# Kernel tuning notes

Hardware: AMD Instinct MI355X
Metric: run time of the kernel (lower is better)

Reference implementation:

```python
import jax, jax.numpy as jnp
import numpy as np

B, S, H = 2, 2048, 2048
NH = 16
Q_LORA, KV_LORA = 1536, 512
D_NOPE, D_ROPE, D_V = 128, 64, 128
D_QK = D_NOPE + D_ROPE
SCALE = 1.0 / np.sqrt(D_QK)
EPS = 1e-6


def _freqs(seq_len):
    # precompute_freqs_cis with scaling_factor=1.0 -> plain RoPE
    inv = 1.0 / (10000.0 ** (np.arange(0, D_ROPE, 2, dtype=np.float32) / D_ROPE))
    t = np.arange(seq_len, dtype=np.float32)
    f = np.outer(t, inv)  # (S, D_ROPE//2)
    return jnp.asarray(np.cos(f)), jnp.asarray(np.sin(f))


def _rope_interleaved(x, cos, sin):
    # x: (B, S, heads, D_ROPE); cos/sin: (S, D_ROPE//2)
    b, s, h, d = x.shape
    xr = x.reshape(b, s, h, d // 2, 2)
    e, o = xr[..., 0], xr[..., 1]
    c = cos[None, :, None, :]
    sn = sin[None, :, None, :]
    re = e * c - o * sn
    im = e * sn + o * c
    return jnp.stack([re, im], axis=-1).reshape(b, s, h, d)


def _rmsnorm(x, w):
    xf = x.astype(jnp.float32)
    rms = jnp.sqrt(jnp.mean(xf * xf, axis=-1, keepdims=True) + EPS)
    return (w * (xf / rms)).astype(x.dtype)


def setup_inputs() -> dict:
    key = jax.random.key(0)
    ks = jax.random.split(key, 6)
    def w(k, shape, fan_in):
        return jax.random.normal(k, shape, dtype=jnp.float32) * (1.0 / np.sqrt(fan_in))
    return {
        "hidden_states": jax.random.normal(ks[0], (B, S, H), dtype=jnp.float32),
        "wq_a": w(ks[1], (Q_LORA, H), H),
        "q_norm_w": jnp.ones((Q_LORA,), dtype=jnp.float32),
        "wq_b": w(ks[2], (NH * D_QK, Q_LORA), Q_LORA),
        "wkv_a": w(ks[3], (KV_LORA + D_ROPE, H), H),
        "kv_norm_w": jnp.ones((KV_LORA,), dtype=jnp.float32),
        "wkv_b": w(ks[4], (NH * (D_NOPE + D_V), KV_LORA), KV_LORA),
        "wo": w(ks[5], (H, NH * D_V), NH * D_V),
    }


def reference(hidden_states, wq_a, q_norm_w, wq_b, wkv_a, kv_norm_w, wkv_b, wo):
    b, s, _ = hidden_states.shape
    cos, sin = _freqs(s)

    # low-rank Q path
    q = hidden_states @ wq_a.T                      # (B,S,Q_LORA)
    q = _rmsnorm(q, q_norm_w)
    q = (q @ wq_b.T).reshape(b, s, NH, D_QK)        # (B,S,NH,192)
    q_nope, q_pe = q[..., :D_NOPE], q[..., D_NOPE:]

    # joint KV compression
    kv = hidden_states @ wkv_a.T                    # (B,S,KV_LORA+D_ROPE)
    kv_c, k_pe = kv[..., :KV_LORA], kv[..., KV_LORA:]
    kv_c = _rmsnorm(kv_c, kv_norm_w)
    k_pe = _rope_interleaved(k_pe[:, :, None, :], cos, sin)  # (B,S,1,64)

    kv_x = (kv_c @ wkv_b.T).reshape(b, s, NH, D_NOPE + D_V)
    k_nope, v = kv_x[..., :D_NOPE], kv_x[..., D_NOPE:]

    q_pe = _rope_interleaved(q_pe, cos, sin)
    qf = jnp.concatenate([q_nope, q_pe], axis=-1)   # (B,S,NH,192)
    kf = jnp.concatenate([k_nope, jnp.broadcast_to(k_pe, (b, s, NH, D_ROPE))], axis=-1)

    scores = jnp.einsum("bqhd,bkhd->bhqk", qf, kf) * SCALE
    attn = jax.nn.softmax(scores.astype(jnp.float32), axis=-1).astype(qf.dtype)
    out = jnp.einsum("bhqk,bkhd->bqhd", attn, v).reshape(b, s, NH * D_V)
    return out @ wo.T
```

## Files before the change

### kernel.cpp

```cpp
#include <hip/hip_runtime.h>
#include <math.h>

#define B_   2
#define S_   2048
#define H_   2048
#define NH_  16
#define T_   (B_*S_)
#define QL   1536
#define KVL  512
#define DN   128
#define DR   64
#define DQK  192
#define DV   128
#define SCALE_ 0.07216878364870323f
#define EPS_ 1e-6f
#define NQKV 2176

typedef unsigned short u16;
typedef __attribute__((ext_vector_type(8))) short bf16x8;
typedef __attribute__((ext_vector_type(4))) float f32x4;

__device__ __forceinline__ u16 f2b(float x) {
  union { float f; unsigned u; } v; v.f = x;
  unsigned r = v.u + 0x7FFFu + ((v.u >> 16) & 1u);
  return (u16)(r >> 16);
}
__device__ __forceinline__ float b2f(u16 u) {
  union { unsigned u; float f; } v; v.u = ((unsigned)u) << 16; return v.f;
}

#define GLD16(src, dst) __builtin_amdgcn_global_load_lds(                       \
    (const __attribute__((address_space(1))) unsigned int*)(src),               \
    (__attribute__((address_space(3))) unsigned int*)(dst), 16, 0, 0)

__device__ __forceinline__ void cvt4(const float* in, u16* out, int i) {
  float4 v = ((const float4*)in)[i];
  u16 r[4] = {f2b(v.x), f2b(v.y), f2b(v.z), f2b(v.w)};
  ((uint2*)out)[i] = *(uint2*)r;
}

__global__ __launch_bounds__(256) void cvt_all(
    const float* __restrict__ hid, const float* __restrict__ wqa,
    const float* __restrict__ wqb, const float* __restrict__ wkva,
    const float* __restrict__ wkvb, const float* __restrict__ wo,
    u16* __restrict__ o_hid, u16* __restrict__ o_wqa, u16* __restrict__ o_wqb,
    u16* __restrict__ o_wkva, u16* __restrict__ o_wkvb, u16* __restrict__ o_wo) {
  int i = blockIdx.x * 256 + threadIdx.x;
  if (i < 2097152) { cvt4(hid, o_hid, i); return; }
  i -= 2097152;
  if (i < 786432) { cvt4(wqa, o_wqa, i); return; }
  i -= 786432;
  if (i < 1179648) { cvt4(wqb, o_wqb, i); return; }
  i -= 1179648;
  if (i < 327680) {
    int row = i >> 9;
    u16 r[4] = {0, 0, 0, 0};
    if (row < 576) {
      float4 v = ((const float4*)wkva)[i];
      r[0] = f2b(v.x); r[1] = f2b(v.y); r[2] = f2b(v.z); r[3] = f2b(v.w);
    }
    ((uint2*)o_wkva)[i] = *(uint2*)r;
    return;
  }
  i -= 327680;
  if (i < 524288) { cvt4(wkvb, o_wkvb, i); return; }
  i -= 524288;
  if (i < 1048576) cvt4(wo, o_wo, i);
}

template <int OUTMODE>
__global__ __launch_bounds__(256) void gemm_mfma(
    const u16* __restrict__ A, int lda,
    const u16* __restrict__ W, int ldw,
    float* __restrict__ Cf, u16* __restrict__ Cb, int ldc,
    int K, float outscale) {
  __shared__ u16 As[4096];
  __shared__ u16 Bs[4096];
  const int tid = threadIdx.x;
  const int wave = tid >> 6, lane = tid & 63, quad = lane >> 4, l16 = lane & 15;
  const int wm = (wave >> 1) * 64, wn = (wave & 1) * 64;
  const size_t m0 = (size_t)blockIdx.y * 128, n0 = (size_t)blockIdx.x * 128;

  f32x4 acc[4][4];
#pragma unroll
  for (int i = 0; i < 4; ++i)
#pragma unroll
    for (int j = 0; j < 4; ++j) acc[i][j] = (f32x4){0.f, 0.f, 0.f, 0.f};

  const int g0 = tid, g1 = tid + 256;
  const u16* a0 = A + (m0 + (g0 >> 6) * 16 + (g0 & 15)) * (size_t)lda + ((g0 >> 4) & 3) * 8;
  const u16* a1 = A + (m0 + (g1 >> 6) * 16 + (g1 & 15)) * (size_t)lda + ((g1 >> 4) & 3) * 8;
  const u16* b0 = W + (n0 + (g0 >> 6) * 16 + (g0 & 15)) * (size_t)ldw + ((g0 >> 4) & 3) * 8;
  const u16* b1 = W + (n0 + (g1 >> 6) * 16 + (g1 & 15)) * (size_t)ldw + ((g1 >> 4) & 3) * 8;

  for (int k0 = 0; k0 < K; k0 += 32) {
    __syncthreads();
    GLD16(a0 + k0, &As[g0 * 8]);
    GLD16(a1 + k0, &As[g1 * 8]);
    GLD16(b0 + k0, &Bs[g0 * 8]);
    GLD16(b1 + k0, &Bs[g1 * 8]);
    __syncthreads();

    bf16x8 af[4], bfr[4];
#pragma unroll
    for (int i = 0; i < 4; ++i)
      af[i] = *(const bf16x8*)&As[((wm >> 4) + i) * 512 + quad * 128 + l16 * 8];
#pragma unroll
    for (int j = 0; j < 4; ++j)
      bfr[j] = *(const bf16x8*)&Bs[((wn >> 4) + j) * 512 + quad * 128 + l16 * 8];
#pragma unroll
    for (int i = 0; i < 4; ++i)
#pragma unroll
      for (int j = 0; j < 4; ++j)
        acc[i][j] = __builtin_amdgcn_mfma_f32_16x16x32_bf16(af[i], bfr[j], acc[i][j], 0, 0, 0);
  }

#pragma unroll
  for (int i = 0; i < 4; ++i)
#pragma unroll
    for (int j = 0; j < 4; ++j)
#pragma unroll
      for (int r = 0; r < 4; ++r) {
        size_t m = m0 + wm + i * 16 + quad * 4 + r;
        size_t n = n0 + wn + j * 16 + l16;
        if (OUTMODE == 0) Cf[m * ldc + n] = acc[i][j][r];
        else              Cb[m * ldc + n] = f2b(acc[i][j][r] * outscale);
      }
}

__global__ __launch_bounds__(256) void rmsnorm_bf(
    const float* __restrict__ x, const float* __restrict__ w,
    u16* __restrict__ o, int D, int sx, int so) {
  const float* p = x + (size_t)blockIdx.x * sx;
  u16* q = o + (size_t)blockIdx.x * so;
  float ss = 0.f;
  for (int i = threadIdx.x; i < D; i += 256) { float v = p[i]; ss += v * v; }
#pragma unroll
  for (int off = 32; off; off >>= 1) ss += __shfl_down(ss, off);
  __shared__ float red[4];
  __shared__ float s_inv;
  if ((threadIdx.x & 63) == 0) red[threadIdx.x >> 6] = ss;
  __syncthreads();
  if (threadIdx.x == 0) {
    float t = red[0] + red[1] + red[2] + red[3];
    s_inv = 1.0f / sqrtf(t / (float)D + EPS_);
  }
  __syncthreads();
  float inv = s_inv;
  for (int i = threadIdx.x; i < D; i += 256) q[i] = f2b(w[i] * p[i] * inv);
}

__global__ void rope_q_bf(u16* __restrict__ Q) {
  int idx = blockIdx.x * blockDim.x + threadIdx.x;
  int pair = idx & 31;
  int head = (idx >> 5) & (NH_ - 1);
  int row = idx >> 9;
  if (row >= T_) return;
  int s = row & (S_ - 1);
  float inv = powf(10000.0f, -(float)(2 * pair) * (1.0f / 64.0f));
  float ang = (float)s * inv;
  float c = cosf(ang), sn = sinf(ang);
  u16* p = Q + (size_t)row * (NH_ * DQK) + head * DQK + DN + 2 * pair;
  unsigned u = *(unsigned*)p;
  float e = b2f((u16)(u & 0xffff)), o = b2f((u16)(u >> 16));
  float re = e * c - o * sn;
  float im = e * sn + o * c;
  *(unsigned*)p = (unsigned)f2b(re) | ((unsigned)f2b(im) << 16);
}

__global__ void kpe_bf_kernel(const float* __restrict__ KVa, u16* __restrict__ KPE) {
  int idx = blockIdx.x * blockDim.x + threadIdx.x;
  int pair = idx & 31;
  int row = idx >> 5;
  if (row >= T_) return;
  int s = row & (S_ - 1);
  float inv = powf(10000.0f, -(float)(2 * pair) * (1.0f / 64.0f));
  float ang = (float)s * inv;
  float c = cosf(ang), sn = sinf(ang);
  const float* p = KVa + (size_t)row * NQKV + 2048 + 2 * pair;
  float e = p[0], o = p[1];
  float re = e * c - o * sn;
  float im = e * sn + o * c;
  *(unsigned*)(KPE + (size_t)row * 64 + 2 * pair) =
      (unsigned)f2b(re) | ((unsigned)f2b(im) << 16);
}

__global__ __launch_bounds__(256) void conv_vt(const u16* __restrict__ KVbf,
                                               u16* __restrict__ Vt) {
  const int h = blockIdx.y, b = blockIdx.z;
  const int s0 = (blockIdx.x >> 1) * 64, d0 = (blockIdx.x & 1) * 64;
  const int t0 = b * S_;
  __shared__ u16 tile[64][72];
  const int tid = threadIdx.x;
#pragma unroll
  for (int i = 0; i < 2; ++i) {
    int c = tid + i * 256;
    int row = c >> 3, off = (c & 7) * 8;
    *(uint4*)&tile[row][off] =
        *(const uint4*)(KVbf + (size_t)(t0 + s0 + row) * 4096 + h * 256 + 128 + d0 + off);
  }
  __syncthreads();
#pragma unroll
  for (int i = 0; i < 2; ++i) {
    int c = tid + i * 256;
    int drow = c >> 3, soff = (c & 7) * 8;
    u16 vals[8];
#pragma unroll
    for (int j = 0; j < 8; ++j) vals[j] = tile[soff + j][drow];
    *(uint4*)(Vt + ((size_t)(b * NH_ + h) * 128 + d0 + drow) * 2048 + s0 + soff) =
        *(uint4*)vals;
  }
}

__global__ __launch_bounds__(512, 4) void flash_mfma(
    const u16* __restrict__ Qbf,
    const u16* __restrict__ KVbf,
    const u16* __restrict__ KPE,
    const u16* __restrict__ Vt,
    u16* __restrict__ Out) {
  const int h = blockIdx.y, b = blockIdx.z;
  const int q0 = blockIdx.x * 128;
  const int t0 = b * S_;
  const int tid = threadIdx.x;
  const int wave = tid >> 6, lane = tid & 63, quad = lane >> 4, l16 = lane & 15;

  __shared__ u16 Ks[2][64 * 192];
  __shared__ u16 Vs[2][128 * 64];

  bf16x8 qf[6];
  {
    const u16* qp = Qbf + (size_t)(t0 + q0 + wave * 16 + l16) * (NH_ * DQK) + h * DQK + quad * 8;
#pragma unroll
    for (int c = 0; c < 6; ++c) qf[c] = *(const bf16x8*)(qp + c * 32);
  }

  const u16* kbase[3]; int kstep[3];
#pragma unroll
  for (int i = 0; i < 3; ++i) {
    int g = i * 512 + tid;
    int r = g & 15, cc = (g >> 4) % 24, kk = (g >> 4) / 24;
    int tok = kk * 16 + r;
    if (cc < 16) { kbase[i] = KVbf + (size_t)(t0 + tok) * 4096 + h * 256 + cc * 8; kstep[i] = 64 * 4096; }
    else         { kbase[i] = KPE + (size_t)(t0 + tok) * 64 + (cc - 16) * 8;       kstep[i] = 64 * 64; }
  }
  const u16* vbase[2];
#pragma unroll
  for (int i = 0; i < 2; ++i) {
    int g = i * 512 + tid;
    int r = g & 15, kc = (g >> 4) & 7, dt = g >> 7;
    vbase[i] = Vt + ((size_t)((b * NH_ + h) * 128) + dt * 16 + r) * 2048 + kc * 8;
  }

  f32x4 of[8];
#pragma unroll
  for (int i = 0; i < 8; ++i) of[i] = (f32x4){0.f, 0.f, 0.f, 0.f};
  float mrun = -3e38f, lrun = 0.f;

#pragma unroll
  for (int i = 0; i < 3; ++i) { GLD16(kbase[i], &Ks[0][(i * 512 + tid) * 8]); kbase[i] += kstep[i]; }
#pragma unroll
  for (int i = 0; i < 2; ++i) GLD16(vbase[i], &Vs[0][(i * 512 + tid) * 8]);

  const int src_lo = (quad & 1) * 32 + l16;
  const int src_hi = src_lo + 16;
  const bool hi_kk = (quad >> 1) != 0;

  for (int it = 0; it < S_ / 64; ++it) {
    const int cur = it & 1;
    __syncthreads();

    if (it + 1 < S_ / 64) {
#pragma unroll
      for (int i = 0; i < 3; ++i) { GLD16(kbase[i], &Ks[cur ^ 1][(i * 512 + tid) * 8]); kbase[i] += kstep[i]; }
#pragma unroll
      for (int i = 0; i < 2; ++i) GLD16(vbase[i] + (it + 1) * 64, &Vs[cur ^ 1][(i * 512 + tid) * 8]);
    }

    f32x4 sc[4];
#pragma unroll
    for (int kk = 0; kk < 4; ++kk) {
      f32x4 s = (f32x4){0.f, 0.f, 0.f, 0.f};
#pragma unroll
      for (int c = 0; c < 6; ++c) {
        bf16x8 kf = *(const bf16x8*)&Ks[cur][((kk * 24 + c * 4 + quad) * 16 + l16) * 8];
        s = __builtin_amdgcn_mfma_f32_16x16x32_bf16(kf, qf[c], s, 0, 0, 0);
      }
      sc[kk] = s;
    }

    float tm = sc[0][0];
#pragma unroll
    for (int kk = 0; kk < 4; ++kk)
#pragma unroll
      for (int r = 0; r < 4; ++r) tm = fmaxf(tm, sc[kk][r]);
    tm = fmaxf(tm, __shfl_xor(tm, 16, 64));
    tm = fmaxf(tm, __shfl_xor(tm, 32, 64));
    float mnew = fmaxf(mrun, tm);
    float alpha = __expf(mrun - mnew);
    mrun = mnew;
    float lsum = 0.f;
#pragma unroll
    for (int kk = 0; kk < 4; ++kk)
#pragma unroll
      for (int r = 0; r < 4; ++r) {
        float p = __expf(sc[kk][r] - mnew);
        sc[kk][r] = p;
        lsum += p;
      }
    lsum += __shfl_xor(lsum, 16, 64);
    lsum += __shfl_xor(lsum, 32, 64);
    lrun = lrun * alpha + lsum;

    unsigned pb[4][2];
#pragma unroll
    for (int kk = 0; kk < 4; ++kk) {
      pb[kk][0] = (unsigned)f2b(sc[kk][0]) | ((unsigned)f2b(sc[kk][1]) << 16);
      pb[kk][1] = (unsigned)f2b(sc[kk][2]) | ((unsigned)f2b(sc[kk][3]) << 16);
    }

    bf16x8 pa[2];
#pragma unroll
    for (int c2 = 0; c2 < 2; ++c2) {
      unsigned a0 = __shfl(pb[c2 * 2][0], src_lo, 64);
      unsigned b0 = __shfl(pb[c2 * 2 + 1][0], src_lo, 64);
      unsigned a1 = __shfl(pb[c2 * 2][1], src_lo, 64);
      unsigned b1 = __shfl(pb[c2 * 2 + 1][1], src_lo, 64);
      unsigned a2 = __shfl(pb[c2 * 2][0], src_hi, 64);
      unsigned b2 = __shfl(pb[c2 * 2 + 1][0], src_hi, 64);
      unsigned a3 = __shfl(pb[c2 * 2][1], src_hi, 64);
      unsigned b3 = __shfl(pb[c2 * 2 + 1][1], src_hi, 64);
      union { unsigned w[4]; bf16x8 v; } u;
      u.w[0] = hi_kk ? b0 : a0;
      u.w[1] = hi_kk ? b1 : a1;
      u.w[2] = hi_kk ? b2 : a2;
      u.w[3] = hi_kk ? b3 : a3;
      pa[c2] = u.v;
    }

#pragma unroll
    for (int dt = 0; dt < 8; ++dt) {
#pragma unroll
      for (int r = 0; r < 4; ++r) of[dt][r] *= alpha;
#pragma unroll
      for (int c2 = 0; c2 < 2; ++c2) {
        bf16x8 vf = *(const bf16x8*)&Vs[cur][((dt * 8 + c2 * 4 + quad) * 16 + l16) * 8];
        of[dt] = __builtin_amdgcn_mfma_f32_16x16x32_bf16(vf, pa[c2], of[dt], 0, 0, 0);
      }
    }
  }

  float inv = 1.0f / lrun;
  u16* op = Out + (size_t)(t0 + q0 + wave * 16 + l16) * (NH_ * DV) + h * DV + quad * 4;
#pragma unroll
  for (int dt = 0; dt < 8; ++dt) {
    u16 r4[4] = {f2b(of[dt][0] * inv), f2b(of[dt][1] * inv),
                 f2b(of[dt][2] * inv), f2b(of[dt][3] * inv)};
    *(uint2*)(op + dt * 16) = *(uint2*)r4;
  }
}

extern "C" void kernel_launch(void* const* d_in, const int* in_sizes, int n_in,
                              void* d_out, int out_size, void* d_ws, size_t ws_size,
                              hipStream_t stream) {
  const float* hidden  = (const float*)d_in[0];
  const float* wq_a    = (const float*)d_in[1];
  const float* q_norm  = (const float*)d_in[2];
  const float* wq_b    = (const float*)d_in[3];
  const float* wkv_a   = (const float*)d_in[4];
  const float* kv_norm = (const float*)d_in[5];
  const float* wkv_b   = (const float*)d_in[6];
  const float* wo      = (const float*)d_in[7];
  float* out = (float*)d_out;

  float* ws = (float*)d_ws;
  u16*   hid_bf  = (u16*)(ws);
  u16*   wqa_bf  = (u16*)(ws + 4194304);
  u16*   wkva_bf = (u16*)(ws + 5767168);
  u16*   wqb_bf  = (u16*)(ws + 6422528);
  u16*   wkvb_bf = (u16*)(ws + 8781824);
  u16*   wo_bf   = (u16*)(ws + 9830400);
  float* qkv_a   = ws + 11927552;
  u16*   attn_bf = (u16*)(ws + 11927552);
  u16*   vt      = (u16*)(ws + 16121856);
  u16*   q_bf    = (u16*)(ws + 22413312);
  u16*   kvn_bf  = (u16*)(ws + 28704768);
  u16*   kpe     = (u16*)(ws + 29753344);
  u16*   kv_bf   = (u16*)(ws + 29884416);
  u16*   qn_bf   = (u16*)(ws + 29884416);
  const size_t need = (size_t)38273024 * sizeof(float);
  if (ws_size < need) return;

  cvt_all<<<23296, 256, 0, stream>>>(hidden, wq_a, wq_b, wkv_a, wkv_b, wo,
                                     hid_bf, wqa_bf, wqb_bf, wkva_bf, wkvb_bf, wo_bf);

  gemm_mfma<0><<<dim3(NQKV / 128, T_ / 128), 256, 0, stream>>>(
      hid_bf, H_, wqa_bf, H_, qkv_a, nullptr, NQKV, H_, 1.0f);

  rmsnorm_bf<<<T_, 256, 0, stream>>>(qkv_a, q_norm, qn_bf, QL, NQKV, QL);
  gemm_mfma<1><<<dim3(NH_ * DQK / 128, T_ / 128), 256, 0, stream>>>(
      qn_bf, QL, wqb_bf, QL, nullptr, q_bf, NH_ * DQK, QL, SCALE_);
  rope_q_bf<<<T_ * NH_ * 32 / 256, 256, 0, stream>>>(q_bf);

  rmsnorm_bf<<<T_, 256, 0, stream>>>(qkv_a + QL, kv_norm, kvn_bf, KVL, NQKV, KVL);
  kpe_bf_kernel<<<T_ * 32 / 256, 256, 0, stream>>>(qkv_a, kpe);
  gemm_mfma<1><<<dim3(NH_ * (DN + DV) / 128, T_ / 128), 256, 0, stream>>>(
      kvn_bf, KVL, wkvb_bf, KVL, nullptr, kv_bf, NH_ * (DN + DV), KVL, 1.0f);
  conv_vt<<<dim3(64, NH_, B_), 256, 0, stream>>>(kv_bf, vt);

  flash_mfma<<<dim3(S_ / 128, NH_, B_), 512, 0, stream>>>(q_bf, kv_bf, kpe, vt, attn_bf);

  gemm_mfma<0><<<dim3(H_ / 128, T_ / 128), 256, 0, stream>>>(
      attn_bf, NH_ * DV, wo_bf, NH_ * DV, out, nullptr, H_, NH_ * DV, 1.0f);
}
```

Measured before the change: 573.1 us.

## Process two query sub-tiles per wave in flash attention with 256-thread blocks

The flash attention kernel now uses 4 waves per block instead of 8, and each wave handles two 16-row query sub-tiles (A and B). Every K and V fragment read from LDS feeds two MFMAs, which halves LDS read traffic per unit of compute. It also adds s_setprio around the MFMA sections and skips the output rescale when no lane's running max changed. The cost is more registers per wave, fewer waves to hide latency, and more global-to-LDS copies per thread.

```diff
diff --git a/kernel.cpp b/kernel.cpp
--- a/kernel.cpp
+++ b/kernel.cpp
@@ -212,7 +212,7 @@
   }
 }
 
-__global__ __launch_bounds__(512, 4) void flash_mfma(
+__global__ __launch_bounds__(256, 2) void flash_mfma(
     const u16* __restrict__ Qbf,
     const u16* __restrict__ KVbf,
     const u16* __restrict__ KPE,
@@ -227,39 +227,47 @@
   __shared__ u16 Ks[2][64 * 192];
   __shared__ u16 Vs[2][128 * 64];
 
-  bf16x8 qf[6];
+  bf16x8 qfA[6], qfB[6];
   {
-    const u16* qp = Qbf + (size_t)(t0 + q0 + wave * 16 + l16) * (NH_ * DQK) + h * DQK + quad * 8;
-#pragma unroll
-    for (int c = 0; c < 6; ++c) qf[c] = *(const bf16x8*)(qp + c * 32);
-  }
-
-  const u16* kbase[3]; int kstep[3];
-#pragma unroll
-  for (int i = 0; i < 3; ++i) {
-    int g = i * 512 + tid;
+    const u16* qpA = Qbf + (size_t)(t0 + q0 + wave * 32 + l16) * (NH_ * DQK) + h * DQK + quad * 8;
+    const u16* qpB = qpA + 16 * (NH_ * DQK);
+#pragma unroll
+    for (int c = 0; c < 6; ++c) {
+      qfA[c] = *(const bf16x8*)(qpA + c * 32);
+      qfB[c] = *(const bf16x8*)(qpB + c * 32);
+    }
+  }
+
+  const u16* kbase[6]; int kstep[6];
+#pragma unroll
+  for (int i = 0; i < 6; ++i) {
+    int g = i * 256 + tid;
     int r = g & 15, cc = (g >> 4) % 24, kk = (g >> 4) / 24;
     int tok = kk * 16 + r;
     if (cc < 16) { kbase[i] = KVbf + (size_t)(t0 + tok) * 4096 + h * 256 + cc * 8; kstep[i] = 64 * 4096; }
     else         { kbase[i] = KPE + (size_t)(t0 + tok) * 64 + (cc - 16) * 8;       kstep[i] = 64 * 64; }
   }
-  const u16* vbase[2];
-#pragma unroll
-  for (int i = 0; i < 2; ++i) {
-    int g = i * 512 + tid;
+  const u16* vbase[4];
+#pragma unroll
+  for (int i = 0; i < 4; ++i) {
+    int g = i * 256 + tid;
     int r = g & 15, kc = (g >> 4) & 7, dt = g >> 7;
     vbase[i] = Vt + ((size_t)((b * NH_ + h) * 128) + dt * 16 + r) * 2048 + kc * 8;
   }
 
-  f32x4 of[8];
-#pragma unroll
-  for (int i = 0; i < 8; ++i) of[i] = (f32x4){0.f, 0.f, 0.f, 0.f};
-  float mrun = -3e38f, lrun = 0.f;
-
-#pragma unroll
-  for (int i = 0; i < 3; ++i) { GLD16(kbase[i], &Ks[0][(i * 512 + tid) * 8]); kbase[i] += kstep[i]; }
-#pragma unroll
-  for (int i = 0; i < 2; ++i) GLD16(vbase[i], &Vs[0][(i * 512 + tid) * 8]);
+  f32x4 ofA[8], ofB[8];
+#pragma unroll
+  for (int i = 0; i < 8; ++i) {
+    ofA[i] = (f32x4){0.f, 0.f, 0.f, 0.f};
+    ofB[i] = (f32x4){0.f, 0.f, 0.f, 0.f};
+  }
+  float mrunA = -3e38f, lrunA = 0.f;
+  float mrunB = -3e38f, lrunB = 0.f;
+
+#pragma unroll
+  for (int i = 0; i < 6; ++i) { GLD16(kbase[i], &Ks[0][(i * 256 + tid) * 8]); kbase[i] += kstep[i]; }
+#pragma unroll
+  for (int i = 0; i < 4; ++i) GLD16(vbase[i], &Vs[0][(i * 256 + tid) * 8]);
 
   const int src_lo = (quad & 1) * 32 + l16;
   const int src_hi = src_lo + 16;
@@ -271,91 +279,170 @@
 
     if (it + 1 < S_ / 64) {
 #pragma unroll
-      for (int i = 0; i < 3; ++i) { GLD16(kbase[i], &Ks[cur ^ 1][(i * 512 + tid) * 8]); kbase[i] += kstep[i]; }
-#pragma unroll
-      for (int i = 0; i < 2; ++i) GLD16(vbase[i] + (it + 1) * 64, &Vs[cur ^ 1][(i * 512 + tid) * 8]);
-    }
-
-    f32x4 sc[4];
+      for (int i = 0; i < 6; ++i) { GLD16(kbase[i], &Ks[cur ^ 1][(i * 256 + tid) * 8]); kbase[i] += kstep[i]; }
+#pragma unroll
+      for (int i = 0; i < 4; ++i) GLD16(vbase[i] + (it + 1) * 64, &Vs[cur ^ 1][(i * 256 + tid) * 8]);
+    }
+
+    __builtin_amdgcn_s_setprio(1);
+    f32x4 scA[4], scB[4];
 #pragma unroll
     for (int kk = 0; kk < 4; ++kk) {
-      f32x4 s = (f32x4){0.f, 0.f, 0.f, 0.f};
+      f32x4 sA = (f32x4){0.f, 0.f, 0.f, 0.f};
+      f32x4 sB = (f32x4){0.f, 0.f, 0.f, 0.f};
 #pragma unroll
       for (int c = 0; c < 6; ++c) {
         bf16x8 kf = *(const bf16x8*)&Ks[cur][((kk * 24 + c * 4 + quad) * 16 + l16) * 8];
-        s = __builtin_amdgcn_mfma_f32_16x16x32_bf16(kf, qf[c], s, 0, 0, 0);
+        sA = __builtin_amdgcn_mfma_f32_16x16x32_bf16(kf, qfA[c], sA, 0, 0, 0);
+        sB = __builtin_amdgcn_mfma_f32_16x16x32_bf16(kf, qfB[c], sB, 0, 0, 0);
       }
-      sc[kk] = s;
-    }
-
-    float tm = sc[0][0];
+      scA[kk] = sA;
+      scB[kk] = sB;
+    }
+    __builtin_amdgcn_s_setprio(0);
+
+    float tmA = scA[0][0];
 #pragma unroll
     for (int kk = 0; kk < 4; ++kk)
 #pragma unroll
-      for (int r = 0; r < 4; ++r) tm = fmaxf(tm, sc[kk][r]);
-    tm = fmaxf(tm, __shfl_xor(tm, 16, 64));
-    tm = fmaxf(tm, __shfl_xor(tm, 32, 64));
-    float mnew = fmaxf(mrun, tm);
-    float alpha = __expf(mrun - mnew);
-    mrun = mnew;
-    float lsum = 0.f;
+      for (int r = 0; r < 4; ++r) tmA = fmaxf(tmA, scA[kk][r]);
+    tmA = fmaxf(tmA, __shfl_xor(tmA, 16, 64));
+    tmA = fmaxf(tmA, __shfl_xor(tmA, 32, 64));
+    const bool upA = __any(tmA > mrunA);
+    float alphaA = 1.f;
+    if (upA) {
+      float mnewA = fmaxf(mrunA, tmA);
+      alphaA = __expf(mrunA - mnewA);
+      mrunA = mnewA;
+    }
+    float lsumA = 0.f;
 #pragma unroll
     for (int kk = 0; kk < 4; ++kk)
 #pragma unroll
       for (int r = 0; r < 4; ++r) {
-        float p = __expf(sc[kk][r] - mnew);
-        sc[kk][r] = p;
-        lsum += p;
+        float p = __expf(scA[kk][r] - mrunA);
+        scA[kk][r] = p;
+        lsumA += p;
       }
-    lsum += __shfl_xor(lsum, 16, 64);
-    lsum += __shfl_xor(lsum, 32, 64);
-    lrun = lrun * alpha + lsum;
-
-    unsigned pb[4][2];
+    lsumA += __shfl_xor(lsumA, 16, 64);
+    lsumA += __shfl_xor(lsumA, 32, 64);
+    lrunA = lrunA * alphaA + lsumA;
+
+    unsigned pbA[4][2];
 #pragma unroll
     for (int kk = 0; kk < 4; ++kk) {
-      pb[kk][0] = (unsigned)f2b(sc[kk][0]) | ((unsigned)f2b(sc[kk][1]) << 16);
-      pb[kk][1] = (unsigned)f2b(sc[kk][2]) | ((unsigned)f2b(sc[kk][3]) << 16);
-    }
-
-    bf16x8 pa[2];
+      pbA[kk][0] = (unsigned)f2b(scA[kk][0]) | ((unsigned)f2b(scA[kk][1]) << 16);
+      pbA[kk][1] = (unsigned)f2b(scA[kk][2]) | ((unsigned)f2b(scA[kk][3]) << 16);
+    }
+    bf16x8 paA[2];
 #pragma unroll
     for (int c2 = 0; c2 < 2; ++c2) {
-      unsigned a0 = __shfl(pb[c2 * 2][0], src_lo, 64);
-      unsigned b0 = __shfl(pb[c2 * 2 + 1][0], src_lo, 64);
-      unsigned a1 = __shfl(pb[c2 * 2][1], src_lo, 64);
-      unsigned b1 = __shfl(pb[c2 * 2 + 1][1], src_lo, 64);
-      unsigned a2 = __shfl(pb[c2 * 2][0], src_hi, 64);
-      unsigned b2 = __shfl(pb[c2 * 2 + 1][0], src_hi, 64);
-      unsigned a3 = __shfl(pb[c2 * 2][1], src_hi, 64);
-      unsigned b3 = __shfl(pb[c2 * 2 + 1][1], src_hi, 64);
+      unsigned a0 = __shfl(pbA[c2 * 2][0], src_lo, 64);
+      unsigned b0 = __shfl(pbA[c2 * 2 + 1][0], src_lo, 64);
+      unsigned a1 = __shfl(pbA[c2 * 2][1], src_lo, 64);
+      unsigned b1 = __shfl(pbA[c2 * 2 + 1][1], src_lo, 64);
+      unsigned a2 = __shfl(pbA[c2 * 2][0], src_hi, 64);
+      unsigned b2 = __shfl(pbA[c2 * 2 + 1][0], src_hi, 64);
+      unsigned a3 = __shfl(pbA[c2 * 2][1], src_hi, 64);
+      unsigned b3 = __shfl(pbA[c2 * 2 + 1][1], src_hi, 64);
       union { unsigned w[4]; bf16x8 v; } u;
       u.w[0] = hi_kk ? b0 : a0;
       u.w[1] = hi_kk ? b1 : a1;
       u.w[2] = hi_kk ? b2 : a2;
       u.w[3] = hi_kk ? b3 : a3;
-      pa[c2] = u.v;
-    }
-
+      paA[c2] = u.v;
+    }
+
+    float tmB = scB[0][0];
+#pragma unroll
+    for (int kk = 0; kk < 4; ++kk)
+#pragma unroll
+      for (int r = 0; r < 4; ++r) tmB = fmaxf(tmB, scB[kk][r]);
+    tmB = fmaxf(tmB, __shfl_xor(tmB, 16, 64));
+    tmB = fmaxf(tmB, __shfl_xor(tmB, 32, 64));
+    const bool upB = __any(tmB > mrunB);
+    float alphaB = 1.f;
+    if (upB) {
+      float mnewB = fmaxf(mrunB, tmB);
+      alphaB = __expf(mrunB - mnewB);
+      mrunB = mnewB;
+    }
+    float lsumB = 0.f;
+#pragma unroll
+    for (int kk = 0; kk < 4; ++kk)
+#pragma unroll
+      for (int r = 0; r < 4; ++r) {
+        float p = __expf(scB[kk][r] - mrunB);
+        scB[kk][r] = p;
+        lsumB += p;
+      }
+    lsumB += __shfl_xor(lsumB, 16, 64);
+    lsumB += __shfl_xor(lsumB, 32, 64);
+    lrunB = lrunB * alphaB + lsumB;
+
+    unsigned pbB[4][2];
+#pragma unroll
+    for (int kk = 0; kk < 4; ++kk) {
+      pbB[kk][0] = (unsigned)f2b(scB[kk][0]) | ((unsigned)f2b(scB[kk][1]) << 16);
+      pbB[kk][1] = (unsigned)f2b(scB[kk][2]) | ((unsigned)f2b(scB[kk][3]) << 16);
+    }
+    bf16x8 paB[2];
+#pragma unroll
+    for (int c2 = 0; c2 < 2; ++c2) {
+      unsigned a0 = __shfl(pbB[c2 * 2][0], src_lo, 64);
+      unsigned b0 = __shfl(pbB[c2 * 2 + 1][0], src_lo, 64);
+      unsigned a1 = __shfl(pbB[c2 * 2][1], src_lo, 64);
+      unsigned b1 = __shfl(pbB[c2 * 2 + 1][1], src_lo, 64);
+      unsigned a2 = __shfl(pbB[c2 * 2][0], src_hi, 64);
+      unsigned b2 = __shfl(pbB[c2 * 2 + 1][0], src_hi, 64);
+      unsigned a3 = __shfl(pbB[c2 * 2][1], src_hi, 64);
+      unsigned b3 = __shfl(pbB[c2 * 2 + 1][1], src_hi, 64);
+      union { unsigned w[4]; bf16x8 v; } u;
+      u.w[0] = hi_kk ? b0 : a0;
+      u.w[1] = hi_kk ? b1 : a1;
+      u.w[2] = hi_kk ? b2 : a2;
+      u.w[3] = hi_kk ? b3 : a3;
+      paB[c2] = u.v;
+    }
+
+    if (upA) {
+#pragma unroll
+      for (int dt = 0; dt < 8; ++dt)
+#pragma unroll
+        for (int r = 0; r < 4; ++r) ofA[dt][r] *= alphaA;
+    }
+    if (upB) {
+#pragma unroll
+      for (int dt = 0; dt < 8; ++dt)
+#pragma unroll
+        for (int r = 0; r < 4; ++r) ofB[dt][r] *= alphaB;
+    }
+
+    __builtin_amdgcn_s_setprio(1);
 #pragma unroll
     for (int dt = 0; dt < 8; ++dt) {
-#pragma unroll
-      for (int r = 0; r < 4; ++r) of[dt][r] *= alpha;
 #pragma unroll
       for (int c2 = 0; c2 < 2; ++c2) {
         bf16x8 vf = *(const bf16x8*)&Vs[cur][((dt * 8 + c2 * 4 + quad) * 16 + l16) * 8];
-        of[dt] = __builtin_amdgcn_mfma_f32_16x16x32_bf16(vf, pa[c2], of[dt], 0, 0, 0);
+        ofA[dt] = __builtin_amdgcn_mfma_f32_16x16x32_bf16(vf, paA[c2], ofA[dt], 0, 0, 0);
+        ofB[dt] = __builtin_amdgcn_mfma_f32_16x16x32_bf16(vf, paB[c2], ofB[dt], 0, 0, 0);
       }
     }
-  }
-
-  float inv = 1.0f / lrun;
-  u16* op = Out + (size_t)(t0 + q0 + wave * 16 + l16) * (NH_ * DV) + h * DV + quad * 4;
+    __builtin_amdgcn_s_setprio(0);
+  }
+
+  float invA = 1.0f / lrunA;
+  float invB = 1.0f / lrunB;
+  u16* opA = Out + (size_t)(t0 + q0 + wave * 32 + l16) * (NH_ * DV) + h * DV + quad * 4;
+  u16* opB = opA + (size_t)16 * (NH_ * DV);
 #pragma unroll
   for (int dt = 0; dt < 8; ++dt) {
-    u16 r4[4] = {f2b(of[dt][0] * inv), f2b(of[dt][1] * inv),
-                 f2b(of[dt][2] * inv), f2b(of[dt][3] * inv)};
-    *(uint2*)(op + dt * 16) = *(uint2*)r4;
+    u16 rA[4] = {f2b(ofA[dt][0] * invA), f2b(ofA[dt][1] * invA),
+                 f2b(ofA[dt][2] * invA), f2b(ofA[dt][3] * invA)};
+    *(uint2*)(opA + dt * 16) = *(uint2*)rA;
+    u16 rB[4] = {f2b(ofB[dt][0] * invB), f2b(ofB[dt][1] * invB),
+                 f2b(ofB[dt][2] * invB), f2b(ofB[dt][3] * invB)};
+    *(uint2*)(opB + dt * 16) = *(uint2*)rB;
   }
 }
 
@@ -407,7 +494,7 @@
       kvn_bf, KVL, wkvb_bf, KVL, nullptr, kv_bf, NH_ * (DN + DV), KVL, 1.0f);
   conv_vt<<<dim3(64, NH_, B_), 256, 0, stream>>>(kv_bf, vt);
 
-  flash_mfma<<<dim3(S_ / 128, NH_, B_), 512, 0, stream>>>(q_bf, kv_bf, kpe, vt, attn_bf);
+  flash_mfma<<<dim3(S_ / 128, NH_, B_), 256, 0, stream>>>(q_bf, kv_bf, kpe, vt, attn_bf);
 
   gemm_mfma<0><<<dim3(H_ / 128, T_ / 128), 256, 0, stream>>>(
       attn_bf, NH_ * DV, wo_bf, NH_ * DV, out, nullptr, H_, NH_ * DV, 1.0f);
```

Result: no change. 583.5 us (+1.8%).

## Single-buffer flash LDS for higher occupancy, lazy rescale, precomputed RoPE table

Applied to the files above, without the earlier changes.

The flash attention kernel drops double-buffered K/V shared memory in favour of a single buffer loaded synchronously each iteration. This halves LDS use, and the launch bound is raised to 8 blocks per CU so more blocks run concurrently and hide latency. MFMA sections are given higher wave priority, and the online softmax skips the output rescale when no running max rises in the wave. A separate kernel precomputes a cos/sin RoPE table so the q and k rope kernels stop evaluating powf, cosf and sinf per element. The trade-off is that global loads no longer overlap compute inside a block, and the higher occupancy bound may cause register spilling.

```diff
diff --git a/kernel.cpp b/kernel.cpp
--- a/kernel.cpp
+++ b/kernel.cpp
@@ -150,16 +150,24 @@
   for (int i = threadIdx.x; i < D; i += 256) q[i] = f2b(w[i] * p[i] * inv);
 }
 
-__global__ void rope_q_bf(u16* __restrict__ Q) {
+__global__ __launch_bounds__(256) void rope_tab_kernel(float* __restrict__ Tab) {
+  int idx = blockIdx.x * 256 + threadIdx.x;
+  int pair = idx & 31;
+  int s = idx >> 5;
+  float inv = powf(10000.0f, -(float)(2 * pair) * (1.0f / 64.0f));
+  float ang = (float)s * inv;
+  ((float2*)Tab)[idx] = make_float2(cosf(ang), sinf(ang));
+}
+
+__global__ void rope_q_bf(u16* __restrict__ Q, const float* __restrict__ Tab) {
   int idx = blockIdx.x * blockDim.x + threadIdx.x;
   int pair = idx & 31;
   int head = (idx >> 5) & (NH_ - 1);
   int row = idx >> 9;
   if (row >= T_) return;
   int s = row & (S_ - 1);
-  float inv = powf(10000.0f, -(float)(2 * pair) * (1.0f / 64.0f));
-  float ang = (float)s * inv;
-  float c = cosf(ang), sn = sinf(ang);
+  float2 cs = ((const float2*)Tab)[(s << 5) | pair];
+  float c = cs.x, sn = cs.y;
   u16* p = Q + (size_t)row * (NH_ * DQK) + head * DQK + DN + 2 * pair;
   unsigned u = *(unsigned*)p;
   float e = b2f((u16)(u & 0xffff)), o = b2f((u16)(u >> 16));
@@ -168,15 +176,15 @@
   *(unsigned*)p = (unsigned)f2b(re) | ((unsigned)f2b(im) << 16);
 }
 
-__global__ void kpe_bf_kernel(const float* __restrict__ KVa, u16* __restrict__ KPE) {
+__global__ void kpe_bf_kernel(const float* __restrict__ KVa, u16* __restrict__ KPE,
+                              const float* __restrict__ Tab) {
   int idx = blockIdx.x * blockDim.x + threadIdx.x;
   int pair = idx & 31;
   int row = idx >> 5;
   if (row >= T_) return;
   int s = row & (S_ - 1);
-  float inv = powf(10000.0f, -(float)(2 * pair) * (1.0f / 64.0f));
-  float ang = (float)s * inv;
-  float c = cosf(ang), sn = sinf(ang);
+  float2 cs = ((const float2*)Tab)[(s << 5) | pair];
+  float c = cs.x, sn = cs.y;
   const float* p = KVa + (size_t)row * NQKV + 2048 + 2 * pair;
   float e = p[0], o = p[1];
   float re = e * c - o * sn;
@@ -212,7 +220,7 @@
   }
 }
 
-__global__ __launch_bounds__(512, 4) void flash_mfma(
+__global__ __launch_bounds__(512, 8) void flash_mfma(
     const u16* __restrict__ Qbf,
     const u16* __restrict__ KVbf,
     const u16* __restrict__ KPE,
@@ -224,8 +232,8 @@
   const int tid = threadIdx.x;
   const int wave = tid >> 6, lane = tid & 63, quad = lane >> 4, l16 = lane & 15;
 
-  __shared__ u16 Ks[2][64 * 192];
-  __shared__ u16 Vs[2][128 * 64];
+  __shared__ u16 Ks[64 * 192];
+  __shared__ u16 Vs[128 * 64];
 
   bf16x8 qf[6];
   {
@@ -256,37 +264,31 @@
   for (int i = 0; i < 8; ++i) of[i] = (f32x4){0.f, 0.f, 0.f, 0.f};
   float mrun = -3e38f, lrun = 0.f;
 
-#pragma unroll
-  for (int i = 0; i < 3; ++i) { GLD16(kbase[i], &Ks[0][(i * 512 + tid) * 8]); kbase[i] += kstep[i]; }
-#pragma unroll
-  for (int i = 0; i < 2; ++i) GLD16(vbase[i], &Vs[0][(i * 512 + tid) * 8]);
-
   const int src_lo = (quad & 1) * 32 + l16;
   const int src_hi = src_lo + 16;
   const bool hi_kk = (quad >> 1) != 0;
 
   for (int it = 0; it < S_ / 64; ++it) {
-    const int cur = it & 1;
     __syncthreads();
-
-    if (it + 1 < S_ / 64) {
-#pragma unroll
-      for (int i = 0; i < 3; ++i) { GLD16(kbase[i], &Ks[cur ^ 1][(i * 512 + tid) * 8]); kbase[i] += kstep[i]; }
-#pragma unroll
-      for (int i = 0; i < 2; ++i) GLD16(vbase[i] + (it + 1) * 64, &Vs[cur ^ 1][(i * 512 + tid) * 8]);
-    }
-
+#pragma unroll
+    for (int i = 0; i < 3; ++i) { GLD16(kbase[i], &Ks[(i * 512 + tid) * 8]); kbase[i] += kstep[i]; }
+#pragma unroll
+    for (int i = 0; i < 2; ++i) GLD16(vbase[i] + it * 64, &Vs[(i * 512 + tid) * 8]);
+    __syncthreads();
+
+    __builtin_amdgcn_s_setprio(1);
     f32x4 sc[4];
 #pragma unroll
     for (int kk = 0; kk < 4; ++kk) {
       f32x4 s = (f32x4){0.f, 0.f, 0.f, 0.f};
 #pragma unroll
       for (int c = 0; c < 6; ++c) {
-        bf16x8 kf = *(const bf16x8*)&Ks[cur][((kk * 24 + c * 4 + quad) * 16 + l16) * 8];
+        bf16x8 kf = *(const bf16x8*)&Ks[((kk * 24 + c * 4 + quad) * 16 + l16) * 8];
         s = __builtin_amdgcn_mfma_f32_16x16x32_bf16(kf, qf[c], s, 0, 0, 0);
       }
       sc[kk] = s;
     }
+    __builtin_amdgcn_s_setprio(0);
 
     float tm = sc[0][0];
 #pragma unroll
@@ -295,15 +297,19 @@
       for (int r = 0; r < 4; ++r) tm = fmaxf(tm, sc[kk][r]);
     tm = fmaxf(tm, __shfl_xor(tm, 16, 64));
     tm = fmaxf(tm, __shfl_xor(tm, 32, 64));
-    float mnew = fmaxf(mrun, tm);
-    float alpha = __expf(mrun - mnew);
-    mrun = mnew;
+    const bool up = __any(tm > mrun);
+    float alpha = 1.f;
+    if (up) {
+      float mnew = fmaxf(mrun, tm);
+      alpha = __expf(mrun - mnew);
+      mrun = mnew;
+    }
     float lsum = 0.f;
 #pragma unroll
     for (int kk = 0; kk < 4; ++kk)
 #pragma unroll
       for (int r = 0; r < 4; ++r) {
-        float p = __expf(sc[kk][r] - mnew);
+        float p = __expf(sc[kk][r] - mrun);
         sc[kk][r] = p;
         lsum += p;
       }
@@ -337,16 +343,23 @@
       pa[c2] = u.v;
     }
 
+    if (up) {
+#pragma unroll
+      for (int dt = 0; dt < 8; ++dt)
+#pragma unroll
+        for (int r = 0; r < 4; ++r) of[dt][r] *= alpha;
+    }
+
+    __builtin_amdgcn_s_setprio(1);
 #pragma unroll
     for (int dt = 0; dt < 8; ++dt) {
 #pragma unroll
-      for (int r = 0; r < 4; ++r) of[dt][r] *= alpha;
-#pragma unroll
       for (int c2 = 0; c2 < 2; ++c2) {
-        bf16x8 vf = *(const bf16x8*)&Vs[cur][((dt * 8 + c2 * 4 + quad) * 16 + l16) * 8];
+        bf16x8 vf = *(const bf16x8*)&Vs[((dt * 8 + c2 * 4 + quad) * 16 + l16) * 8];
         of[dt] = __builtin_amdgcn_mfma_f32_16x16x32_bf16(vf, pa[c2], of[dt], 0, 0, 0);
       }
     }
+    __builtin_amdgcn_s_setprio(0);
   }
 
   float inv = 1.0f / lrun;
@@ -382,6 +395,7 @@
   float* qkv_a   = ws + 11927552;
   u16*   attn_bf = (u16*)(ws + 11927552);
   u16*   vt      = (u16*)(ws + 16121856);
+  float* rope_tab = ws + 20840448;
   u16*   q_bf    = (u16*)(ws + 22413312);
   u16*   kvn_bf  = (u16*)(ws + 28704768);
   u16*   kpe     = (u16*)(ws + 29753344);
@@ -393,16 +407,18 @@
   cvt_all<<<23296, 256, 0, stream>>>(hidden, wq_a, wq_b, wkv_a, wkv_b, wo,
                                      hid_bf, wqa_bf, wqb_bf, wkva_bf, wkvb_bf, wo_bf);
 
+  rope_tab_kernel<<<S_ * 32 / 256, 256, 0, stream>>>(rope_tab);
+
   gemm_mfma<0><<<dim3(NQKV / 128, T_ / 128), 256, 0, stream>>>(
       hid_bf, H_, wqa_bf, H_, qkv_a, nullptr, NQKV, H_, 1.0f);
 
   rmsnorm_bf<<<T_, 256, 0, stream>>>(qkv_a, q_norm, qn_bf, QL, NQKV, QL);
   gemm_mfma<1><<<dim3(NH_ * DQK / 128, T_ / 128), 256, 0, stream>>>(
       qn_bf, QL, wqb_bf, QL, nullptr, q_bf, NH_ * DQK, QL, SCALE_);
-  rope_q_bf<<<T_ * NH_ * 32 / 256, 256, 0, stream>>>(q_bf);
+  rope_q_bf<<<T_ * NH_ * 32 / 256, 256, 0, stream>>>(q_bf, rope_tab);
 
   rmsnorm_bf<<<T_, 256, 0, stream>>>(qkv_a + QL, kv_norm, kvn_bf, KVL, NQKV, KVL);
-  kpe_bf_kernel<<<T_ * 32 / 256, 256, 0, stream>>>(qkv_a, kpe);
+  kpe_bf_kernel<<<T_ * 32 / 256, 256, 0, stream>>>(qkv_a, kpe, rope_tab);
   gemm_mfma<1><<<dim3(NH_ * (DN + DV) / 128, T_ / 128), 256, 0, stream>>>(
       kvn_bf, KVL, wkvb_bf, KVL, nullptr, kv_bf, NH_ * (DN + DV), KVL, 1.0f);
   conv_vt<<<dim3(64, NH_, B_), 256, 0, stream>>>(kv_bf, vt);
```

Measured after the change: 922.5 us. 61.0% more time.
